# Performance work log

Measured on AMD Instinct MI355X. Metric: run time of the kernel, lower is better.

The kernel has to match this reference:

```python
import jax, jax.numpy as jnp
import numpy as np

K = 32
MAX_ITER = 30
STOP_COND = 1e-07
TIE_EPS = 1e-08


def _all_dist(C, X):
    # squared Euclidean distance matrix: (B, N, K)
    xx = jnp.sum(X * X, axis=-1)[:, :, None]      # (B, N, 1)
    cc = jnp.sum(C * C, axis=-1)[:, None, :]      # (B, 1, K)
    xc = jnp.einsum('bnd,bkd->bnk', X, C)         # (B, N, K)
    return cc + xx - 2.0 * xc


def setup_inputs() -> dict:
    key = jax.random.key(0)
    k1, k2 = jax.random.split(key)
    E = jax.random.normal(k1, (4, 8192, 64), dtype=jnp.float32)
    log_W = jax.random.normal(k2, (4, 8192), dtype=jnp.float32)
    return {"E": E, "log_W": log_W}


def reference(E, log_W):
    B, N, D = E.shape
    key = jax.random.key(42)
    k_init, k_loop = jax.random.split(key)

    # sel_vectors: random K distinct points as initial centroids
    sel = jax.random.permutation(k_init, N)[:K]
    C0 = E[:, sel, :]                              # (B, K, D)
    ass0 = jnp.zeros((B, N, K), dtype=E.dtype)
    done0 = jnp.array(False)

    def step(carry, it):
        C, ass, X, done = carry
        Dm = _all_dist(C, X)                       # (B, N, K)
        mind = jnp.min(Dm, axis=2)                 # (B, N)
        ass_new = (jnp.abs(Dm - mind[:, :, None]) < TIE_EPS).astype(X.dtype)
        df = jnp.sum(jnp.abs(ass_new - ass), axis=(1, 2)) / N   # (B,)
        done_now = done | jnp.all(df < STOP_COND)

        # soft weighting over members of each cluster (exp of log_W, masked)
        aw = ass_new * log_W[:, :, None] - 100.0 * (1.0 - ass_new)
        aw = aw - jnp.max(aw, axis=1, keepdims=True)
        aw = jnp.exp(aw) * ass_new                 # (B, N, K)
        ass_fat = jnp.sum(aw, axis=1, keepdims=True)   # (B, 1, K)
        ass_norm = aw / jnp.clip(ass_fat, 1e-12, None)

        # empty-cluster handling: replace data rows at empty-cluster indices
        # with random data points (mirrors in-place X mutation in torch code)
        kk = jax.random.fold_in(k_loop, it)
        repl_idx = jax.random.randint(kk, (X.shape[0], K), 0, N)
        repl = jnp.take_along_axis(X, repl_idx[:, :, None], axis=1)  # (B, K, D)
        empty = (ass_fat[:, 0, :] == 0)[:, :, None]                  # (B, K, 1)
        X_new = X.at[:, :K, :].set(jnp.where(empty, repl, X[:, :K, :]))

        C_new = jnp.einsum('bnk,bnd->bkd', ass_norm, X_new)

        # freeze state once converged (torch breaks before updating ass/C)
        C = jnp.where(done_now, C, C_new)
        ass = jnp.where(done_now, ass, ass_new)
        X = jnp.where(done_now, X, X_new)
        return (C, ass, X, done_now), None

    (C, ass, X, _), _ = jax.lax.scan(step, (C0, ass0, E, done0), jnp.arange(MAX_ITER))

    # final stats
    Dm = _all_dist(C, X)
    mind = jnp.min(Dm, axis=2)                     # (B, N)
    obj = jnp.mean(mind, axis=1)                   # (B,)
    mind_rep = jnp.min(Dm, axis=1)                 # (B, K)
    rep_idx = jnp.argmin(Dm, axis=1)               # (B, K)
    ass_rep = (jnp.abs(Dm - mind_rep[:, None, :]) < TIE_EPS).astype(X.dtype)
    ass_rep = ass_rep / jnp.clip(jnp.sum(ass_rep, axis=1, keepdims=True), 0.001, None)
    rep = jnp.einsum('bnk,bnd->bkd', ass_rep, X)   # (B, K, D)

    return ass, C, rep, rep_idx, obj
```

## Files before the change

### kernel.cpp

```cpp
#include <hip/hip_runtime.h>
#include <stdint.h>

typedef unsigned int u32;
typedef unsigned long long u64;

#define Bb 4
#define Nn 8192
#define Dd 64
#define Kk 32
#define MAXIT 30
#define NBLK 256
#define RPB  64

#define ACC_STRIDE 2112

enum : u32 {
  WS_BAR   = 0u,
  WS_SEL   = 64u,
  WS_MASKH = 192u,
  WS_C0    = 1280u,
  WS_XHEAD = 34048u,
  WS_KEYS1 = 66816u,
  WS_KEYS2 = 99584u,
  WS_A1K   = 132352u,
  WS_A1V   = 165120u,
  WS_A2K   = 197888u,
  WS_A2V   = 230656u,
  WS_ACC   = 263424u,
  WS_CHG   = 364800u,
  WS_POBJ  = 364864u,
  WS_PMIN  = 365888u,
  WS_DM    = 431424u
};

__device__ __forceinline__ void tf2x32(u32 k0, u32 k1, u32 x0, u32 x1, u32& o0, u32& o1){
  u32 ks2 = k0 ^ k1 ^ 0x1BD11BDAu;
  x0 += k0; x1 += k1;
#define TFR(r) { x0 += x1; x1 = (x1<<(r))|(x1>>(32-(r))); x1 ^= x0; }
  TFR(13) TFR(15) TFR(26) TFR(6)
  x0 += k1;  x1 += ks2 + 1u;
  TFR(17) TFR(29) TFR(16) TFR(24)
  x0 += ks2; x1 += k0 + 2u;
  TFR(13) TFR(15) TFR(26) TFR(6)
  x0 += k0;  x1 += k1 + 3u;
  TFR(17) TFR(29) TFR(16) TFR(24)
  x0 += k1;  x1 += ks2 + 4u;
  TFR(13) TFR(15) TFR(26) TFR(6)
  x0 += ks2; x1 += k0 + 5u;
#undef TFR
  o0 = x0; o1 = x1;
}

__global__ __launch_bounds__(1024, 1) void kinit(const float* __restrict__ E, char* __restrict__ ws){
  const int tid = threadIdx.x;
  u32* bar   = (u32*)(ws + WS_BAR);
  u32* sel   = (u32*)(ws + WS_SEL);
  u32* keys1 = (u32*)(ws + WS_KEYS1);
  u32* keys2 = (u32*)(ws + WS_KEYS2);
  u32* a1k = (u32*)(ws + WS_A1K); u32* a1v = (u32*)(ws + WS_A1V);
  u32* a2k = (u32*)(ws + WS_A2K); u32* a2v = (u32*)(ws + WS_A2V);
  float* C0 = (float*)(ws + WS_C0);
  float* XH = (float*)(ws + WS_XHEAD);
  float* ACC0 = (float*)(ws + WS_ACC);
  float* CHG  = (float*)(ws + WS_CHG);

  __shared__ u32 hist[8192];
  __shared__ u32 lsum[1024];
  __shared__ u32 sel_s[32];

  if (tid < 4) bar[tid] = 0u;
  if (tid < 3) CHG[tid] = 0.f;
  for (int i = tid; i < Bb*ACC_STRIDE; i += 1024) ACC0[i] = 0.f;

  u32 i0,i1; tf2x32(0u,42u, 0u,0u, i0,i1);
  u32 key10,key11, s10,s11;
  tf2x32(i0,i1, 0u,0u, key10,key11);
  tf2x32(i0,i1, 0u,1u, s10,s11);
  u32 s20,s21; tf2x32(key10,key11, 0u,1u, s20,s21);

  for (int i = tid; i < 8192; i += 1024){
    u32 y0,y1;
    tf2x32(s10,s11, 0u,(u32)i, y0,y1); keys1[i] = y0 ^ y1;
    tf2x32(s20,s21, 0u,(u32)i, y0,y1); keys2[i] = y0 ^ y1;
  }
  for (int i = tid; i < 8192; i += 1024){
    int b = i >> 11; int rem = i & 2047;
    XH[i] = E[(size_t)b*Nn*Dd + rem];
  }
  __syncthreads();

  for (int rnd = 0; rnd < 2; rnd++){
    u32* keys = rnd ? keys2 : keys1;
    u32* ak   = rnd ? a2k   : a1k;
    u32* av   = rnd ? a2v   : a1v;
    for (int i = tid; i < 8192; i += 1024) hist[i] = 0u;
    __syncthreads();
    for (int i = tid; i < 8192; i += 1024) atomicAdd(&hist[keys[i]>>19], 1u);
    __syncthreads();
    { u32 s = 0;
      for (int j = 0; j < 8; j++) s += hist[tid*8+j];
      lsum[tid] = s; }
    __syncthreads();
    for (int st = 1; st < 1024; st <<= 1){
      u32 v = (tid >= st) ? lsum[tid-st] : 0u;
      __syncthreads();
      lsum[tid] += v;
      __syncthreads();
    }
    { u32 run = tid ? lsum[tid-1] : 0u;
      for (int j = 0; j < 8; j++){ u32 c = hist[tid*8+j]; hist[tid*8+j] = run; run += c; } }
    __syncthreads();
    for (int i = tid; i < 8192; i += 1024){
      u32 kx = keys[i];
      u32 pos = atomicAdd(&hist[kx>>19], 1u);
      ak[pos] = kx; av[pos] = (u32)i;
    }
    __syncthreads();
    for (int bkt = tid; bkt < 8192; bkt += 1024){
      int s0 = bkt ? (int)hist[bkt-1] : 0;
      int e0 = (int)hist[bkt];
      for (int i = s0+1; i < e0; i++){
        u32 kx = ak[i], vx = av[i];
        int j = i-1;
        while (j >= s0 && (ak[j] > kx || (ak[j] == kx && av[j] > vx))){
          ak[j+1] = ak[j]; av[j+1] = av[j]; j--;
        }
        ak[j+1] = kx; av[j+1] = vx;
      }
    }
    __syncthreads();
  }
  if (tid < 32){ u32 p = a2v[tid]; u32 sj = a1v[p]; sel[tid] = sj; sel_s[tid] = sj; }
  __syncthreads();
  for (int i = tid; i < 8192; i += 1024){
    int b = i >> 11; int k = (i >> 6) & 31; int d = i & 63;
    C0[i] = E[(size_t)b*Nn*Dd + (size_t)sel_s[k]*Dd + d];
  }
}

__device__ __forceinline__ void grid_barrier(u32* bar){
  __syncthreads();
  if (threadIdx.x == 0){
    u32 g = __hip_atomic_load(&bar[1], __ATOMIC_RELAXED, __HIP_MEMORY_SCOPE_AGENT);
    u32 a = __hip_atomic_fetch_add(&bar[0], 1u, __ATOMIC_RELEASE, __HIP_MEMORY_SCOPE_AGENT);
    if (a == (u32)(NBLK-1)){
      __hip_atomic_store(&bar[0], 0u, __ATOMIC_RELAXED, __HIP_MEMORY_SCOPE_AGENT);
      __hip_atomic_store(&bar[1], g + 1u, __ATOMIC_RELEASE, __HIP_MEMORY_SCOPE_AGENT);
    } else {
      int polls = 0;
      for (;;){
        u32 v = __hip_atomic_load(&bar[1], __ATOMIC_RELAXED, __HIP_MEMORY_SCOPE_AGENT);
        if (v != g) break;
        if ((++polls & 63) == 0){
          v = __hip_atomic_load(&bar[1], __ATOMIC_ACQUIRE, __HIP_MEMORY_SCOPE_AGENT);
          if (v != g) break;
        }
        __builtin_amdgcn_s_sleep(2);
      }
    }
    __builtin_amdgcn_fence(__ATOMIC_ACQUIRE, "agent");
  }
  __syncthreads();
}

#define CALC_XXH() do { float s0=0.f,s1=0.f,s2=0.f,s3=0.f; \
  _Pragma("unroll") \
  for (int j=0;j<4;j++){ s0+=x[4*j]*x[4*j]; s1+=x[4*j+1]*x[4*j+1]; s2+=x[4*j+2]*x[4*j+2]; s3+=x[4*j+3]*x[4*j+3]; } \
  xxh=(s0+s1)+(s2+s3); } while(0)

#define CALC_DIST() do { \
  float xxf = xxh + __shfl_xor(xxh, 1); \
  xxf += __shfl_xor(xxf, 2); \
  _Pragma("unroll") \
  for (int k=0;k<32;k++){ \
    const float4* cp = (const float4*)&Cl[k*64 + h*16]; \
    float s0=0.f,s1=0.f,s2=0.f,s3=0.f; \
    _Pragma("unroll") \
    for (int j=0;j<4;j++){ float4 c = cp[j]; s0+=x[4*j]*c.x; s1+=x[4*j+1]*c.y; s2+=x[4*j+2]*c.z; s3+=x[4*j+3]*c.w; } \
    float dot=(s0+s1)+(s2+s3); \
    dot += __shfl_xor(dot, 1); \
    dot += __shfl_xor(dot, 2); \
    dloc[k]=(ccl[k]+xxf)-2.f*dot; \
  } } while(0)

__global__ __launch_bounds__(512, 1) void kmain(const float* __restrict__ E, const float* __restrict__ LW,
                                                float* __restrict__ out, char* __restrict__ ws){
  const int tid = threadIdx.x;
  const int bid = blockIdx.x;
  const int b   = bid >> 6;
  const int r   = bid & 63;
  const int h   = tid & 3;
  const int pl  = tid >> 2;
  const int n   = (r << 7) + pl;

  u32*   bar   = (u32*)(ws + WS_BAR);
  u32*   maskh = (u32*)(ws + WS_MASKH);
  float* C0    = (float*)(ws + WS_C0);
  float* XH    = (float*)(ws + WS_XHEAD);
  float* ACC   = (float*)(ws + WS_ACC);
  float* CHG   = (float*)(ws + WS_CHG);
  float* Pobj  = (float*)(ws + WS_POBJ);
  u64*   Pmin  = (u64*)(ws + WS_PMIN);
  float* Dm    = (float*)(ws + WS_DM);

  __shared__ float Cl[2048];
  __shared__ float ccl[32];
  __shared__ float part[ACC_STRIDE];
  __shared__ float newX[2048];
  __shared__ u64   kminl[32];
  __shared__ float red[512];
  __shared__ u32   sh_empty, sh_idx, sh_tcnt;
  __shared__ float sh_chgf, sh_mind;

  float x[16]; float xxh;
  { const float4* xr = (const float4*)(E + (size_t)(b*Nn + n)*Dd + h*16);
    #pragma unroll
    for (int j=0;j<4;j++){ float4 v = xr[j]; x[4*j]=v.x; x[4*j+1]=v.y; x[4*j+2]=v.z; x[4*j+3]=v.w; } }
  CALC_XXH();
  const float w = expf(LW[b*Nn + n]);

  u32 kl0, kl1; tf2x32(0u,42u, 0u,1u, kl0, kl1);

  for (int i = tid; i < 2048; i += 512) Cl[i] = C0[b*2048 + i];
  __syncthreads();
  if (tid < 32){ float s=0.f; const float* cr=&Cl[tid*64];
    #pragma unroll
    for (int d2=0; d2<64; d2++) s += cr[d2]*cr[d2];
    ccl[tid]=s; }
  __syncthreads();

  u32 prevmask = 0u;
  float dloc[32];

  for (int it = 0; it < MAXIT; it++){
    const int par = it & 1;
    const int cur = it % 3, nxt = (it + 1) % 3;
    CALC_DIST();
    float mind = dloc[0];
    #pragma unroll
    for (int k=1;k<32;k++) mind = fminf(mind, dloc[k]);
    u32 mask = 0u;
    #pragma unroll
    for (int k=0;k<32;k++) if (fabsf(dloc[k]-mind) < 1e-8f) mask |= (1u<<k);
    int changed = (h==0) ? ((it==0) ? 1 : (mask != prevmask)) : 0;
    prevmask = mask;
    if (r == 0 && tid < 128 && h == 0) maskh[par*128 + b*32 + pl] = mask;

    __syncthreads();
    for (int i = tid; i < ACC_STRIDE; i += 512) part[i] = 0.f;
    __syncthreads();
    { u32 mm = mask;
      while (mm){
        int k = __ffs(mm) - 1; mm &= mm - 1;
        #pragma unroll
        for (int d2=0; d2<16; d2++) atomicAdd(&part[(h*16 + d2)*32 + k], w*x[d2]);
        if (h == 0){
          atomicAdd(&part[2048 + k], w);
          atomicAdd(&part[2080 + k], 1.0f);
        }
      } }
    int nchg = __syncthreads_count(changed);
    { float* dst = ACC + (size_t)cur*Bb*ACC_STRIDE + b*ACC_STRIDE;
      for (int i = tid; i < ACC_STRIDE; i += 512) unsafeAtomicAdd(&dst[i], part[i]);
      if (tid == 0 && nchg) unsafeAtomicAdd(&CHG[cur], (float)nchg);
      float* nz = ACC + (size_t)nxt*Bb*ACC_STRIDE + b*ACC_STRIDE;
      if (tid < 33) nz[r*33 + tid] = 0.f;
      if (b == 0 && r == 0 && tid == 33) CHG[nxt] = 0.f;
    }
    grid_barrier(bar);

    { const float* src = ACC + (size_t)cur*Bb*ACC_STRIDE;
      for (int i = tid; i < ACC_STRIDE; i += 512) part[i] = src[b*ACC_STRIDE + i];
      float cv = 1.f;
      if (tid < 128) cv = src[(tid >> 5)*ACC_STRIDE + 2080 + (tid & 31)];
      if (tid == 0) sh_chgf = CHG[cur];
      int anyempty = __syncthreads_or(cv == 0.f);
      if (sh_chgf == 0.f) break;

      { bool e = (tid < 32) && (part[2080 + tid] == 0.f);
        u64 bal = __ballot(e);
        if (tid == 0) sh_empty = (u32)bal; }
      __syncthreads();
      u32 em = sh_empty;

      if (anyempty){
        u32 g0, g1; tf2x32(kl0, kl1, 0u, (u32)it, g0, g1);
        for (int k = 0; k < 32; k++){
          if (!((em >> k) & 1u)) continue;
          int j = b*32 + k;
          u32 y0, y1; tf2x32(g0, g1, 0u, (u32)j, y0, y1);
          u32 ridx = (y0 ^ y1) & 8191u;
          u32 mj = maskh[par*128 + b*32 + k];
          float wj = expf(LW[b*Nn + k]);
          if (tid < 64){
            float xo = XH[(b*32 + k)*64 + tid];
            float xn = (ridx < 32u) ? XH[(b*32 + (int)ridx)*64 + tid]
                                    : E[(size_t)(b*Nn + (int)ridx)*Dd + tid];
            newX[k*64 + tid] = xn;
            float dxw = wj * (xn - xo);
            u32 m2 = mj;
            while (m2){ int kq = __ffs(m2) - 1; m2 &= m2 - 1; part[tid*32 + kq] += dxw; }
          }
        }
        __syncthreads();
        grid_barrier(bar);
        if (r == 0){
          for (int k = 0; k < 32; k++){
            if (!((em >> k) & 1u)) continue;
            if (tid < 64) XH[(b*32 + k)*64 + tid] = newX[k*64 + tid];
          }
          __syncthreads();
          if (tid < 128 && ((em >> pl) & 1u)){
            #pragma unroll
            for (int d2 = 0; d2 < 16; d2++) x[d2] = newX[pl*64 + h*16 + d2];
            CALC_XXH();
          }
        }
      }
    }
    __syncthreads();
    for (int i = tid; i < 2048; i += 512){
      int k = i >> 6, d = i & 63;
      Cl[i] = part[d*32 + k] / fmaxf(part[2048 + k], 1e-12f);
    }
    __syncthreads();
    if (tid < 32){ float s=0.f; const float* cr=&Cl[tid*64];
      #pragma unroll
      for (int d2=0; d2<64; d2++) s += cr[d2]*cr[d2];
      ccl[tid]=s; }
    __syncthreads();
  }

  CALC_DIST();
  float mind = dloc[0];
  #pragma unroll
  for (int k=1;k<32;k++) mind = fminf(mind, dloc[k]);
  #pragma unroll
  for (int kq=0;kq<8;kq++){
    int k = h*8 + kq;
    Dm[(size_t)(b*32 + k)*Nn + n] = dloc[k];
  }
  { float4* dst = (float4*)(out + (size_t)(b*Nn + n)*32);
    #pragma unroll
    for (int qq=0;qq<2;qq++){
      int q = h*2 + qq;
      float4 v;
      v.x = ((prevmask>>(4*q  ))&1u) ? 1.f : 0.f;
      v.y = ((prevmask>>(4*q+1))&1u) ? 1.f : 0.f;
      v.z = ((prevmask>>(4*q+2))&1u) ? 1.f : 0.f;
      v.w = ((prevmask>>(4*q+3))&1u) ? 1.f : 0.f;
      dst[q] = v;
    } }
  if (tid < 32) kminl[tid] = ~0ull;
  red[tid] = (h==0) ? mind : 0.f;
  __syncthreads();
  #pragma unroll
  for (int kq=0;kq<8;kq++){
    int k = h*8 + kq;
    u32 u = __float_as_uint(dloc[k]);
    u = (u & 0x80000000u) ? ~u : (u | 0x80000000u);
    u64 pk = ((u64)u << 32) | (u32)n;
    atomicMin(&kminl[k], pk);
  }
  for (int s2 = 256; s2 > 0; s2 >>= 1){
    if (tid < s2) red[tid] += red[tid + s2];
    __syncthreads();
  }
  if (tid < 32) Pmin[(size_t)(b*32 + tid)*64 + r] = kminl[tid];
  if (tid == 0) Pobj[b*64 + r] = red[0];
  grid_barrier(bar);

  if (bid < 128){
    const int b2 = bid >> 5, k2 = bid & 31;
    const size_t OFF_C    = (size_t)Bb*Nn*Kk;
    const size_t OFF_REP  = OFF_C + (size_t)Bb*Kk*Dd;
    const size_t OFF_RIDX = OFF_REP + (size_t)Bb*Kk*Dd;
    const size_t OFF_OBJ  = OFF_RIDX + (size_t)Bb*Kk;
    if (tid == 0){
      u64 m = ~0ull;
      for (int bl = 0; bl < 64; bl++){ u64 v = Pmin[(size_t)(b2*32 + k2)*64 + bl]; if (v < m) m = v; }
      u32 enc = (u32)(m >> 32);
      u32 ub  = (enc & 0x80000000u) ? (enc & 0x7fffffffu) : ~enc;
      sh_mind = __uint_as_float(ub);
      sh_idx  = (u32)(m & 0xffffffffu);
      sh_tcnt = 0u;
    }
    if (tid < 64) newX[tid] = 0.f;
    __syncthreads();
    float mr = sh_mind;
    for (int nn = tid; nn < Nn; nn += 512){
      float dv = Dm[(size_t)(b2*32 + k2)*Nn + nn];
      if (fabsf(dv - mr) < 1e-8f){
        atomicAdd(&sh_tcnt, 1u);
        const float* xr = (nn < 32) ? &XH[(b2*32 + nn)*64] : &E[(size_t)(b2*Nn + nn)*Dd];
        for (int d2 = 0; d2 < 64; d2++) atomicAdd(&newX[d2], xr[d2]);
      }
    }
    __syncthreads();
    if (tid < 64){
      out[OFF_C   + (size_t)(b2*32 + k2)*64 + tid] = Cl[k2*64 + tid];
      out[OFF_REP + (size_t)(b2*32 + k2)*64 + tid] = newX[tid] / (float)sh_tcnt;
    }
    if (tid == 0) out[OFF_RIDX + b2*32 + k2] = (float)sh_idx;
    if (k2 == 0){
      if (tid < 64) red[tid] = Pobj[b2*64 + tid];
      __syncthreads();
      if (tid == 0){ float s = 0.f; for (int i2 = 0; i2 < 64; i2++) s += red[i2];
        out[OFF_OBJ + b2] = s / (float)Nn; }
    }
  }
}

extern "C" void kernel_launch(void* const* d_in, const int* in_sizes, int n_in,
                              void* d_out, int out_size, void* d_ws, size_t ws_size,
                              hipStream_t stream) {
  const float* E  = (const float*)d_in[0];
  const float* LW = (const float*)d_in[1];
  float* out = (float*)d_out;
  char*  ws  = (char*)d_ws;
  (void)in_sizes; (void)n_in; (void)out_size; (void)ws_size;
  kinit<<<dim3(1),    dim3(1024), 0, stream>>>(E, ws);
  kmain<<<dim3(NBLK), dim3(512),  0, stream>>>(E, LW, out, ws);
}
```

Baseline: 1.212 ms.

## Parallelize permutation-based centroid init across persistent grid with grid barriers

Moves the random-permutation sort (threefry key generation, bucket histogram, scan, scatter, per-bucket insertion sort) out of a single-block init kernel into the persistent main kernel, spreading the work over all 256 blocks with four extra grid barriers. The init kernel shrinks to zeroing the global histograms, accumulators and barrier state. This removes a long serial single-block phase before the main loop, at the cost of extra grid-wide synchronisation and global atomics on histograms.

```diff
diff --git a/kernel.cpp b/kernel.cpp
--- a/kernel.cpp
+++ b/kernel.cpp
@@ -11,14 +11,13 @@
 #define MAXIT 30
 #define NBLK 256
 #define RPB  64
+#define NTH  512
 
 #define ACC_STRIDE 2112
 
 enum : u32 {
   WS_BAR   = 0u,
-  WS_SEL   = 64u,
   WS_MASKH = 192u,
-  WS_C0    = 1280u,
   WS_XHEAD = 34048u,
   WS_KEYS1 = 66816u,
   WS_KEYS2 = 99584u,
@@ -30,7 +29,9 @@
   WS_CHG   = 364800u,
   WS_POBJ  = 364864u,
   WS_PMIN  = 365888u,
-  WS_DM    = 431424u
+  WS_DM    = 431424u,
+  WS_HIST1 = 4625728u,
+  WS_HIST2 = 4658496u
 };
 
 __device__ __forceinline__ void tf2x32(u32 k0, u32 k1, u32 x0, u32 x1, u32& o0, u32& o1){
@@ -51,91 +52,17 @@
   o0 = x0; o1 = x1;
 }
 
-__global__ __launch_bounds__(1024, 1) void kinit(const float* __restrict__ E, char* __restrict__ ws){
+__global__ __launch_bounds__(1024, 1) void kzero(char* __restrict__ ws){
   const int tid = threadIdx.x;
   u32* bar   = (u32*)(ws + WS_BAR);
-  u32* sel   = (u32*)(ws + WS_SEL);
-  u32* keys1 = (u32*)(ws + WS_KEYS1);
-  u32* keys2 = (u32*)(ws + WS_KEYS2);
-  u32* a1k = (u32*)(ws + WS_A1K); u32* a1v = (u32*)(ws + WS_A1V);
-  u32* a2k = (u32*)(ws + WS_A2K); u32* a2v = (u32*)(ws + WS_A2V);
-  float* C0 = (float*)(ws + WS_C0);
-  float* XH = (float*)(ws + WS_XHEAD);
+  float* CHG = (float*)(ws + WS_CHG);
   float* ACC0 = (float*)(ws + WS_ACC);
-  float* CHG  = (float*)(ws + WS_CHG);
-
-  __shared__ u32 hist[8192];
-  __shared__ u32 lsum[1024];
-  __shared__ u32 sel_s[32];
-
+  u32* h1 = (u32*)(ws + WS_HIST1);
+  u32* h2 = (u32*)(ws + WS_HIST2);
   if (tid < 4) bar[tid] = 0u;
   if (tid < 3) CHG[tid] = 0.f;
   for (int i = tid; i < Bb*ACC_STRIDE; i += 1024) ACC0[i] = 0.f;
-
-  u32 i0,i1; tf2x32(0u,42u, 0u,0u, i0,i1);
-  u32 key10,key11, s10,s11;
-  tf2x32(i0,i1, 0u,0u, key10,key11);
-  tf2x32(i0,i1, 0u,1u, s10,s11);
-  u32 s20,s21; tf2x32(key10,key11, 0u,1u, s20,s21);
-
-  for (int i = tid; i < 8192; i += 1024){
-    u32 y0,y1;
-    tf2x32(s10,s11, 0u,(u32)i, y0,y1); keys1[i] = y0 ^ y1;
-    tf2x32(s20,s21, 0u,(u32)i, y0,y1); keys2[i] = y0 ^ y1;
-  }
-  for (int i = tid; i < 8192; i += 1024){
-    int b = i >> 11; int rem = i & 2047;
-    XH[i] = E[(size_t)b*Nn*Dd + rem];
-  }
-  __syncthreads();
-
-  for (int rnd = 0; rnd < 2; rnd++){
-    u32* keys = rnd ? keys2 : keys1;
-    u32* ak   = rnd ? a2k   : a1k;
-    u32* av   = rnd ? a2v   : a1v;
-    for (int i = tid; i < 8192; i += 1024) hist[i] = 0u;
-    __syncthreads();
-    for (int i = tid; i < 8192; i += 1024) atomicAdd(&hist[keys[i]>>19], 1u);
-    __syncthreads();
-    { u32 s = 0;
-      for (int j = 0; j < 8; j++) s += hist[tid*8+j];
-      lsum[tid] = s; }
-    __syncthreads();
-    for (int st = 1; st < 1024; st <<= 1){
-      u32 v = (tid >= st) ? lsum[tid-st] : 0u;
-      __syncthreads();
-      lsum[tid] += v;
-      __syncthreads();
-    }
-    { u32 run = tid ? lsum[tid-1] : 0u;
-      for (int j = 0; j < 8; j++){ u32 c = hist[tid*8+j]; hist[tid*8+j] = run; run += c; } }
-    __syncthreads();
-    for (int i = tid; i < 8192; i += 1024){
-      u32 kx = keys[i];
-      u32 pos = atomicAdd(&hist[kx>>19], 1u);
-      ak[pos] = kx; av[pos] = (u32)i;
-    }
-    __syncthreads();
-    for (int bkt = tid; bkt < 8192; bkt += 1024){
-      int s0 = bkt ? (int)hist[bkt-1] : 0;
-      int e0 = (int)hist[bkt];
-      for (int i = s0+1; i < e0; i++){
-        u32 kx = ak[i], vx = av[i];
-        int j = i-1;
-        while (j >= s0 && (ak[j] > kx || (ak[j] == kx && av[j] > vx))){
-          ak[j+1] = ak[j]; av[j+1] = av[j]; j--;
-        }
-        ak[j+1] = kx; av[j+1] = vx;
-      }
-    }
-    __syncthreads();
-  }
-  if (tid < 32){ u32 p = a2v[tid]; u32 sj = a1v[p]; sel[tid] = sj; sel_s[tid] = sj; }
-  __syncthreads();
-  for (int i = tid; i < 8192; i += 1024){
-    int b = i >> 11; int k = (i >> 6) & 31; int d = i & 63;
-    C0[i] = E[(size_t)b*Nn*Dd + (size_t)sel_s[k]*Dd + d];
-  }
+  for (int i = tid; i < 8192; i += 1024){ h1[i] = 0u; h2[i] = 0u; }
 }
 
 __device__ __forceinline__ void grid_barrier(u32* bar){
@@ -195,8 +122,13 @@
 
   u32*   bar   = (u32*)(ws + WS_BAR);
   u32*   maskh = (u32*)(ws + WS_MASKH);
-  float* C0    = (float*)(ws + WS_C0);
   float* XH    = (float*)(ws + WS_XHEAD);
+  u32*   keys1 = (u32*)(ws + WS_KEYS1);
+  u32*   keys2 = (u32*)(ws + WS_KEYS2);
+  u32*   a1k   = (u32*)(ws + WS_A1K); u32* a1v = (u32*)(ws + WS_A1V);
+  u32*   a2k   = (u32*)(ws + WS_A2K); u32* a2v = (u32*)(ws + WS_A2V);
+  u32*   hist1 = (u32*)(ws + WS_HIST1);
+  u32*   hist2 = (u32*)(ws + WS_HIST2);
   float* ACC   = (float*)(ws + WS_ACC);
   float* CHG   = (float*)(ws + WS_CHG);
   float* Pobj  = (float*)(ws + WS_POBJ);
@@ -209,8 +141,81 @@
   __shared__ float newX[2048];
   __shared__ u64   kminl[32];
   __shared__ float red[512];
+  __shared__ u32   scan[512];
+  __shared__ u32   sel_s[32];
   __shared__ u32   sh_empty, sh_idx, sh_tcnt;
   __shared__ float sh_chgf, sh_mind;
+
+  {
+    const int g = bid*NTH + tid;
+    if (g < 8192){
+      u32 i0,i1; tf2x32(0u,42u, 0u,0u, i0,i1);
+      u32 key10,key11, s10,s11;
+      tf2x32(i0,i1, 0u,0u, key10,key11);
+      tf2x32(i0,i1, 0u,1u, s10,s11);
+      u32 s20,s21; tf2x32(key10,key11, 0u,1u, s20,s21);
+      u32 y0,y1;
+      tf2x32(s10,s11, 0u,(u32)g, y0,y1); u32 k1x = y0 ^ y1;
+      tf2x32(s20,s21, 0u,(u32)g, y0,y1); u32 k2x = y0 ^ y1;
+      keys1[g] = k1x; keys2[g] = k2x;
+      atomicAdd(&hist1[k1x>>19], 1u);
+      atomicAdd(&hist2[k2x>>19], 1u);
+      XH[g] = E[(size_t)(g>>11)*Nn*Dd + (size_t)(g & 2047)];
+    }
+  }
+  grid_barrier(bar);
+  if (bid < 2){
+    u32* hh = bid ? hist2 : hist1;
+    u32 loc[16]; u32 s = 0;
+    #pragma unroll
+    for (int j = 0; j < 16; j++){ loc[j] = hh[tid*16 + j]; s += loc[j]; }
+    scan[tid] = s;
+    __syncthreads();
+    for (int st = 1; st < 512; st <<= 1){
+      u32 v = (tid >= st) ? scan[tid - st] : 0u;
+      __syncthreads();
+      scan[tid] += v;
+      __syncthreads();
+    }
+    u32 run = tid ? scan[tid-1] : 0u;
+    #pragma unroll
+    for (int j = 0; j < 16; j++){ u32 c = loc[j]; hh[tid*16 + j] = run; run += c; }
+  }
+  grid_barrier(bar);
+  {
+    const int g = bid*NTH + tid;
+    if (g < 8192){
+      u32 kx = keys1[g];
+      u32 pos = atomicAdd(&hist1[kx>>19], 1u);
+      a1k[pos] = kx; a1v[pos] = (u32)g;
+      kx = keys2[g];
+      pos = atomicAdd(&hist2[kx>>19], 1u);
+      a2k[pos] = kx; a2v[pos] = (u32)g;
+    }
+  }
+  grid_barrier(bar);
+  if (tid < 64){
+    int g2 = bid*32 + (tid & 31);
+    u32* ak = (tid < 32) ? a1k : a2k;
+    u32* av = (tid < 32) ? a1v : a2v;
+    u32* hh = (tid < 32) ? hist1 : hist2;
+    int s0 = g2 ? (int)hh[g2-1] : 0;
+    int e0 = (int)hh[g2];
+    for (int i2 = s0+1; i2 < e0; i2++){
+      u32 kx = ak[i2], vx = av[i2];
+      int j = i2-1;
+      while (j >= s0 && (ak[j] > kx || (ak[j] == kx && av[j] > vx))){
+        ak[j+1] = ak[j]; av[j+1] = av[j]; j--;
+      }
+      ak[j+1] = kx; av[j+1] = vx;
+    }
+  }
+  grid_barrier(bar);
+  if (tid < 32){ u32 p = a2v[tid]; sel_s[tid] = a1v[p]; }
+  __syncthreads();
+  for (int i = tid; i < 2048; i += NTH){
+    Cl[i] = E[(size_t)b*Nn*Dd + (size_t)sel_s[i>>6]*Dd + (i & 63)];
+  }
 
   float x[16]; float xxh;
   { const float4* xr = (const float4*)(E + (size_t)(b*Nn + n)*Dd + h*16);
@@ -221,7 +226,6 @@
 
   u32 kl0, kl1; tf2x32(0u,42u, 0u,1u, kl0, kl1);
 
-  for (int i = tid; i < 2048; i += 512) Cl[i] = C0[b*2048 + i];
   __syncthreads();
   if (tid < 32){ float s=0.f; const float* cr=&Cl[tid*64];
     #pragma unroll
@@ -419,6 +423,6 @@
   float* out = (float*)d_out;
   char*  ws  = (char*)d_ws;
   (void)in_sizes; (void)n_in; (void)out_size; (void)ws_size;
-  kinit<<<dim3(1),    dim3(1024), 0, stream>>>(E, ws);
+  kzero<<<dim3(1),    dim3(1024), 0, stream>>>(ws);
   kmain<<<dim3(NBLK), dim3(512),  0, stream>>>(E, LW, out, ws);
 }
```

After: 1.185 ms. 2.2% less time.
